# Performance work log

Hardware: AMD Instinct MI355X
Metric: run time of the kernel (lower is better)

The kernel has to match this reference:

```python
import jax, jax.numpy as jnp
import numpy as np

RES = 128          # image / k-space resolution
DECIMATION = 4     # acceleration factor
P = RES * RES // DECIMATION  # 4096 trajectory points
B = 8              # batch


def setup_inputs() -> dict:
    key = jax.random.key(0)
    k1, k2 = jax.random.split(key)
    k_space_input = jax.random.normal(k1, (B, 1, RES, RES, 2), dtype=jnp.float32)
    # learnable k-space trajectory in pixel units, range [-RES/2, RES/2]
    trajectory = (jax.random.uniform(k2, (P, 2), dtype=jnp.float32) - 0.5) * RES
    return {"k_space_input": k_space_input, "trajectory": trajectory}


def _grid_sample_points(img, pts_norm):
    """torch.nn.functional.grid_sample (bilinear, zero padding, align_corners=False)
    evaluated at a list of points.
    img: (B, C, H, W); pts_norm: (P, 2) in [-1, 1], [:, 0] -> x (W axis), [:, 1] -> y (H axis).
    Returns (B, C, P)."""
    H, W = img.shape[-2], img.shape[-1]
    x = (pts_norm[:, 0] + 1.0) * (W * 0.5) - 0.5
    y = (pts_norm[:, 1] + 1.0) * (H * 0.5) - 0.5
    x0f = jnp.floor(x)
    y0f = jnp.floor(y)
    wx = x - x0f  # differentiable interpolation weights
    wy = y - y0f
    x0 = x0f.astype(jnp.int32)
    y0 = y0f.astype(jnp.int32)

    def tap(ix, iy, w):
        valid = ((ix >= 0) & (ix < W) & (iy >= 0) & (iy < H)).astype(img.dtype)
        ixc = jnp.clip(ix, 0, W - 1)
        iyc = jnp.clip(iy, 0, H - 1)
        return img[:, :, iyc, ixc] * (w * valid)  # (B, C, P)

    return (tap(x0, y0, (1 - wx) * (1 - wy))
            + tap(x0 + 1, y0, wx * (1 - wy))
            + tap(x0, y0 + 1, (1 - wx) * wy)
            + tap(x0 + 1, y0 + 1, wx * wy))


def _forward(k_space_input, trajectory):
    # (B,1,H,W,2) -> (B,2,H,W): channels = (real, imag)
    ksp = jnp.transpose(k_space_input, (0, 1, 4, 2, 3))[:, 0]
    # bilinear resampling of cartesian k-space at the trajectory points
    pts = trajectory / (RES * 0.5)  # normalize to [-1, 1] as in the torch helper
    sub = _grid_sample_points(ksp, pts)            # (B, 2, P)
    c = sub[:, 0] + 1j * sub[:, 1]                 # complex measurements (B, P)
    # adjoint (type-1) NUFFT back to a centered RES x RES image grid:
    # img[y, x] = (1/RES) * sum_p c[p] * exp(+2*pi*i*(ky_p*y + kx_p*x)/RES)
    xs = jnp.arange(RES, dtype=jnp.float32) - RES * 0.5  # centered grid coords
    phase = (2.0 * jnp.pi / RES)
    Ax = jnp.exp(1j * phase * trajectory[:, 0][:, None] * xs[None, :])  # (P, W)
    Ay = jnp.exp(1j * phase * trajectory[:, 1][:, None] * xs[None, :])  # (P, H)
    tmp = c[:, :, None] * Ay[None, :, :]           # (B, P, H)
    img = jnp.einsum('bph,pw->bhw', tmp, Ax) / RES  # (B, H, W), 1/sqrt(H*W) scale
    out = jnp.stack([img.real, img.imag], axis=-1)[:, None]  # (B, 1, H, W, 2)
    return out


def reference(k_space_input, trajectory):
    return _forward(k_space_input, trajectory)
```

## Files before the change

kernel.cpp:

```cpp
#include <hip/hip_runtime.h>

#define RES    128
#define P_PTS  4096
#define CHUNKS 32
#define PP     128

typedef _Float16 half8  __attribute__((ext_vector_type(8)));
typedef _Float16 half2v __attribute__((ext_vector_type(2)));
typedef float    f32x4  __attribute__((ext_vector_type(4)));

__global__ __launch_bounds__(256) void gemm_kernel(const float* __restrict__ ksp,
                                                   const float* __restrict__ traj,
                                                   half2v* __restrict__ part) {
    __shared__ float2 st[PP];
    __shared__ float2 sc[PP];
    __shared__ __align__(16) _Float16 sA[4096];
    __shared__ __align__(16) _Float16 sB[8192];

    const int chunk = blockIdx.x;
    const int b     = blockIdx.y >> 1;
    const int mh    = blockIdx.y & 1;
    const int tid   = threadIdx.x;
    const int wave  = tid >> 6;
    const int lane  = tid & 63;
    const int l15   = lane & 15;
    const int q     = lane >> 4;

    if (tid < PP) {
        const int p = chunk * PP + tid;
        const float tx = traj[2 * p], ty = traj[2 * p + 1];
        st[tid] = make_float2(tx, ty);
        const float x = tx + 63.5f, y = ty + 63.5f;
        const float x0f = floorf(x), y0f = floorf(y);
        const float wx = x - x0f, wy = y - y0f;
        const int ix0 = (int)x0f, iy0 = (int)y0f;
        float re = 0.0f, im = 0.0f;
#pragma unroll
        for (int dy = 0; dy < 2; ++dy) {
#pragma unroll
            for (int dx = 0; dx < 2; ++dx) {
                const int ix = ix0 + dx, iy = iy0 + dy;
                const float w = (dx ? wx : 1.0f - wx) * (dy ? wy : 1.0f - wy);
                if (ix >= 0 && ix < RES && iy >= 0 && iy < RES) {
                    const float2 v = *(const float2*)(ksp + ((b * RES + iy) * RES + ix) * 2);
                    re = fmaf(v.x, w, re);
                    im = fmaf(v.y, w, im);
                }
            }
        }
        sc[tid] = make_float2(re * (1.0f / 128.0f), im * (1.0f / 128.0f));
    }
    __syncthreads();

    f32x4 accR[4][2], accI[4][2];
#pragma unroll
    for (int i = 0; i < 4; ++i)
#pragma unroll
        for (int j = 0; j < 2; ++j) {
            accR[i][j] = (f32x4){0.f, 0.f, 0.f, 0.f};
            accI[i][j] = (f32x4){0.f, 0.f, 0.f, 0.f};
        }

    const float inv = 1.0f / 128.0f;
    const int nB = tid & 127, kB = tid >> 7;
    const int mA = tid & 63,  kA = tid >> 6;
    const float xn = ((float)nB - 64.0f) * inv;
    const float xm = ((float)(mh * 64 + mA) - 64.0f) * inv;

    for (int r = 0; r < 4; ++r) {
        const int p0 = r * 32;
#pragma unroll
        for (int i = 0; i < 4; ++i) {
            const int k8l = kB + 2 * i;
            half8 v;
#pragma unroll
            for (int j = 0; j < 4; ++j) {
                const int pl = p0 + k8l * 4 + j;
                const float rev = st[pl].x * xn;
                const float f = rev - floorf(rev);
                v[2 * j]     = (_Float16)__builtin_amdgcn_cosf(f);
                v[2 * j + 1] = (_Float16)__builtin_amdgcn_sinf(f);
            }
            *(half8*)(sB + ((size_t)(k8l * 128 + nB)) * 8) = v;
        }
#pragma unroll
        for (int i = 0; i < 2; ++i) {
            const int k8l = kA + 4 * i;
            half8 v;
#pragma unroll
            for (int j = 0; j < 4; ++j) {
                const int pl = p0 + k8l * 4 + j;
                const float rev = st[pl].y * xm;
                const float f = rev - floorf(rev);
                const float cs = __builtin_amdgcn_cosf(f);
                const float sn = __builtin_amdgcn_sinf(f);
                const float cr = sc[pl].x, ci = sc[pl].y;
                v[2 * j]     = (_Float16)(cr * cs - ci * sn);
                v[2 * j + 1] = (_Float16)(cr * sn + ci * cs);
            }
            *(half8*)(sA + ((size_t)(k8l * 64 + mA)) * 8) = v;
        }
        __syncthreads();

        const half8 SGN = {(_Float16)1.f, (_Float16)-1.f, (_Float16)1.f, (_Float16)-1.f,
                           (_Float16)1.f, (_Float16)-1.f, (_Float16)1.f, (_Float16)-1.f};
#pragma unroll
        for (int s = 0; s < 2; ++s) {
            const _Float16* pa = sA + (s * 4 + q) * 512;
            const _Float16* pb = sB + (s * 4 + q) * 1024;
            half8 an[4], b1[2], b2[2];
#pragma unroll
            for (int mt = 0; mt < 4; ++mt)
                an[mt] = *(const half8*)(pa + (mt * 16 + l15) * 8);
#pragma unroll
            for (int nt = 0; nt < 2; ++nt) {
                const half8 bv = *(const half8*)(pb + (wave * 32 + nt * 16 + l15) * 8);
                b1[nt] = bv * SGN;
                b2[nt] = __builtin_shufflevector(bv, bv,
                                                 1, 0, 3, 2, 5, 4, 7, 6);
            }
#pragma unroll
            for (int mt = 0; mt < 4; ++mt)
#pragma unroll
                for (int nt = 0; nt < 2; ++nt) {
                    accR[mt][nt] = __builtin_amdgcn_mfma_f32_16x16x32_f16(
                        an[mt], b1[nt], accR[mt][nt], 0, 0, 0);
                    accI[mt][nt] = __builtin_amdgcn_mfma_f32_16x16x32_f16(
                        an[mt], b2[nt], accI[mt][nt], 0, 0, 0);
                }
        }
        __syncthreads();
    }

#pragma unroll
    for (int mt = 0; mt < 4; ++mt) {
#pragma unroll
        for (int nt = 0; nt < 2; ++nt) {
            const int n = wave * 32 + nt * 16 + l15;
#pragma unroll
            for (int rg = 0; rg < 4; ++rg) {
                const int m = b * 128 + mh * 64 + mt * 16 + q * 4 + rg;
                half2v pv;
                pv[0] = (_Float16)accR[mt][nt][rg];
                pv[1] = (_Float16)accI[mt][nt][rg];
                part[(size_t)chunk * 131072 + m * 128 + n] = pv;
            }
        }
    }
}

__global__ __launch_bounds__(256) void reduce_kernel(const half8* __restrict__ part,
                                                     f32x4* __restrict__ out) {
    const int i = blockIdx.x * 256 + threadIdx.x;
    float s[8];
#pragma unroll
    for (int k = 0; k < 8; ++k) s[k] = 0.f;
#pragma unroll
    for (int c = 0; c < CHUNKS; ++c) {
        const half8 v = part[(size_t)c * 32768 + i];
#pragma unroll
        for (int k = 0; k < 8; ++k) s[k] += (float)v[k];
    }
    f32x4 lo = {s[0], s[1], s[2], s[3]};
    f32x4 hi = {s[4], s[5], s[6], s[7]};
    out[2 * i]     = lo;
    out[2 * i + 1] = hi;
}

extern "C" void kernel_launch(void* const* d_in, const int* in_sizes, int n_in,
                              void* d_out, int out_size, void* d_ws, size_t ws_size,
                              hipStream_t stream) {
    const float* ksp  = (const float*)d_in[0];
    const float* traj = (const float*)d_in[1];
    half2v* part = (half2v*)d_ws;

    hipLaunchKernelGGL(gemm_kernel,   dim3(CHUNKS, 16), dim3(256), 0, stream,
                       ksp, traj, part);
    hipLaunchKernelGGL(reduce_kernel, dim3(128),        dim3(256), 0, stream,
                       (const half8*)part, (f32x4*)d_out);
}
```

Baseline: 74.98 us.

## Replace partial-sum buffer and reduce kernel with float atomics into output

Result: slower. 93.02 us (+24.1%).

```diff
diff --git a/kernel.cpp b/kernel.cpp
--- a/kernel.cpp
+++ b/kernel.cpp
@@ -2,16 +2,15 @@
 
 #define RES    128
 #define P_PTS  4096
-#define CHUNKS 32
-#define PP     128
+#define CHUNKS 16
+#define PP     256
 
 typedef _Float16 half8  __attribute__((ext_vector_type(8)));
-typedef _Float16 half2v __attribute__((ext_vector_type(2)));
 typedef float    f32x4  __attribute__((ext_vector_type(4)));
 
 __global__ __launch_bounds__(256) void gemm_kernel(const float* __restrict__ ksp,
                                                    const float* __restrict__ traj,
-                                                   half2v* __restrict__ part) {
+                                                   float* __restrict__ out) {
     __shared__ float2 st[PP];
     __shared__ float2 sc[PP];
     __shared__ __align__(16) _Float16 sA[4096];
@@ -26,7 +25,7 @@
     const int l15   = lane & 15;
     const int q     = lane >> 4;
 
-    if (tid < PP) {
+    {
         const int p = chunk * PP + tid;
         const float tx = traj[2 * p], ty = traj[2 * p + 1];
         st[tid] = make_float2(tx, ty);
@@ -67,7 +66,7 @@
     const float xn = ((float)nB - 64.0f) * inv;
     const float xm = ((float)(mh * 64 + mA) - 64.0f) * inv;
 
-    for (int r = 0; r < 4; ++r) {
+    for (int r = 0; r < 8; ++r) {
         const int p0 = r * 32;
 #pragma unroll
         for (int i = 0; i < 4; ++i) {
@@ -140,31 +139,12 @@
 #pragma unroll
             for (int rg = 0; rg < 4; ++rg) {
                 const int m = b * 128 + mh * 64 + mt * 16 + q * 4 + rg;
-                half2v pv;
-                pv[0] = (_Float16)accR[mt][nt][rg];
-                pv[1] = (_Float16)accI[mt][nt][rg];
-                part[(size_t)chunk * 131072 + m * 128 + n] = pv;
+                float* dst = out + ((size_t)(m * 128 + n)) * 2;
+                unsafeAtomicAdd(dst,     accR[mt][nt][rg]);
+                unsafeAtomicAdd(dst + 1, accI[mt][nt][rg]);
             }
         }
     }
-}
-
-__global__ __launch_bounds__(256) void reduce_kernel(const half8* __restrict__ part,
-                                                     f32x4* __restrict__ out) {
-    const int i = blockIdx.x * 256 + threadIdx.x;
-    float s[8];
-#pragma unroll
-    for (int k = 0; k < 8; ++k) s[k] = 0.f;
-#pragma unroll
-    for (int c = 0; c < CHUNKS; ++c) {
-        const half8 v = part[(size_t)c * 32768 + i];
-#pragma unroll
-        for (int k = 0; k < 8; ++k) s[k] += (float)v[k];
-    }
-    f32x4 lo = {s[0], s[1], s[2], s[3]};
-    f32x4 hi = {s[4], s[5], s[6], s[7]};
-    out[2 * i]     = lo;
-    out[2 * i + 1] = hi;
 }
 
 extern "C" void kernel_launch(void* const* d_in, const int* in_sizes, int n_in,
@@ -172,10 +152,8 @@
                               hipStream_t stream) {
     const float* ksp  = (const float*)d_in[0];
     const float* traj = (const float*)d_in[1];
-    half2v* part = (half2v*)d_ws;
 
-    hipLaunchKernelGGL(gemm_kernel,   dim3(CHUNKS, 16), dim3(256), 0, stream,
-                       ksp, traj, part);
-    hipLaunchKernelGGL(reduce_kernel, dim3(128),        dim3(256), 0, stream,
-                       (const half8*)part, (f32x4*)d_out);
+    hipMemsetAsync(d_out, 0, (size_t)8 * 128 * 128 * 2 * sizeof(float), stream);
+    hipLaunchKernelGGL(gemm_kernel, dim3(CHUNKS, 16), dim3(256), 0, stream,
+                       ksp, traj, (float*)d_out);
 }
```
